# Kernel tuning notes

Measured on AMD Instinct MI355X. Metric: run time of the kernel, lower is better.

Reference implementation:

```python
import jax, jax.numpy as jnp
import numpy as np


def setup_inputs() -> dict:
    key = jax.random.key(0)
    ks = jax.random.split(key, 6)
    B, C, H, W = 4, 256, 64, 64
    C8 = C // 8
    s = 0.05
    return {
        "x": jax.random.normal(ks[0], (B, C, H, W), dtype=jnp.float32),
        "Wf": jax.random.normal(ks[1], (C8, C), dtype=jnp.float32) * s,
        "bf": jnp.zeros((C8,), dtype=jnp.float32),
        "Wg": jax.random.normal(ks[2], (C8, C), dtype=jnp.float32) * s,
        "bg": jnp.zeros((C8,), dtype=jnp.float32),
        "Wh": jax.random.normal(ks[3], (C, C), dtype=jnp.float32) * s,
        "bh": jnp.zeros((C,), dtype=jnp.float32),
        "gamma": jnp.ones((1,), dtype=jnp.float32),
    }


def reference(x, Wf, bf, Wg, bg, Wh, bh, gamma):
    B, C, H, W = x.shape
    N = H * W
    xf = x.reshape(B, C, N)  # [B, C, N] (1x1 conv == matmul over channels)
    f = jnp.einsum("kc,bcn->bkn", Wf, xf) + bf[None, :, None]  # [B, C/8, N]
    g = jnp.einsum("kc,bcn->bkn", Wg, xf) + bg[None, :, None]  # [B, C/8, N]
    h = jnp.einsum("oc,bcn->bon", Wh, xf) + bh[None, :, None]  # [B, C, N]
    # attention_map[b, n, m] = sum_k f[b,k,n] * g[b,k,m]  (f^T g)
    attn = jnp.einsum("bkn,bkm->bnm", f, g)  # [B, N, N]
    # softmax over dim -2 (the f-position axis), as in the torch module
    attn = jax.nn.softmax(attn, axis=-2)
    # out[b,c,m] = sum_n h[b,c,n] * attn[b,n,m]
    out = jnp.einsum("bcn,bnm->bcm", h, attn).reshape(B, C, H, W)
    return gamma * out + x
```

## Files before the change

### kernel.cpp

```cpp
#include <hip/hip_runtime.h>
#include <hip/hip_bf16.h>
#include <hip/hip_fp16.h>

typedef __attribute__((ext_vector_type(8))) short short8;
typedef __attribute__((ext_vector_type(8))) _Float16 half8;
typedef __attribute__((ext_vector_type(4))) float f32x4;
typedef __attribute__((ext_vector_type(16))) float f32x16;
typedef __attribute__((ext_vector_type(4))) unsigned int uint4v;
typedef unsigned short u16;
typedef unsigned int u32;

#define LOG2E 1.44269504088896f

typedef const void __attribute__((address_space(1))) gvoid;
typedef void __attribute__((address_space(3))) lvoid;

__device__ __forceinline__ void gll16(const void* g, void* l) {
  __builtin_amdgcn_global_load_lds((gvoid*)g, (lvoid*)l, 16, 0, 0);
}

__device__ __forceinline__ u16 f2bf(float f) {
  u32 u = __builtin_bit_cast(u32, f);
  u += 0x7fffu + ((u >> 16) & 1u);
  return (u16)(u >> 16);
}
__device__ __forceinline__ u16 f2h(float f) {
  _Float16 h = (_Float16)f;
  return __builtin_bit_cast(u16, h);
}
__device__ __forceinline__ u32 cvtpk_bf16(float lo, float hi) {
  u32 r;
  asm("v_cvt_pk_bf16_f32 %0, %1, %2" : "=v"(r) : "v"(lo), "v"(hi));
  return r;
}

__global__ void k_prep(const float* __restrict__ x,
                       const float* __restrict__ Wf, const float* __restrict__ bfp,
                       const float* __restrict__ Wg, const float* __restrict__ bgp,
                       const float* __restrict__ Wh, const float* __restrict__ bhp,
                       u16* __restrict__ xT, u16* __restrict__ Wall,
                       float* __restrict__ ball)
{
  int bid = blockIdx.x, t = threadIdx.x;
  if (bid < 1024) {
    __shared__ u16 tile[64][68];
    int b = bid >> 8, c0 = ((bid >> 6) & 3) << 6, n0 = (bid & 63) << 6;
#pragma unroll
    for (int r = 0; r < 4; ++r) {
      int cl = (t >> 4) + r * 16, nl = (t & 15) * 4;
      const float4 v = *(const float4*)&x[(size_t)(b * 256 + c0 + cl) * 4096 + n0 + nl];
      tile[cl][nl + 0] = f2h(v.x); tile[cl][nl + 1] = f2h(v.y);
      tile[cl][nl + 2] = f2h(v.z); tile[cl][nl + 3] = f2h(v.w);
    }
    __syncthreads();
#pragma unroll
    for (int r = 0; r < 4; ++r) {
      int nl = (t >> 4) + r * 16, cl = (t & 15) * 4;
      ushort4 o;
      o.x = tile[cl + 0][nl]; o.y = tile[cl + 1][nl];
      o.z = tile[cl + 2][nl]; o.w = tile[cl + 3][nl];
      *(ushort4*)&xT[(size_t)(b * 4096 + n0 + nl) * 256 + c0 + cl] = o;
    }
  } else {
    int wb = bid - 1024;
    int e = wb * 1024 + t * 4;
    int r = e >> 8;
    const float* src = (r < 32) ? (Wf + e)
                     : (r < 64) ? (Wg + e - 32 * 256)
                                : (Wh + e - 64 * 256);
    float4 v = *(const float4*)src;
    float sc = (r >= 32 && r < 64) ? LOG2E : 1.0f;
    ushort4 o;
    o.x = f2h(v.x * sc); o.y = f2h(v.y * sc);
    o.z = f2h(v.z * sc); o.w = f2h(v.w * sc);
    *(ushort4*)&Wall[e] = o;
    if (wb == 0 && t < 80) {
#pragma unroll
      for (int i = 0; i < 4; ++i) {
        int idx = t * 4 + i;
        ball[idx] = (idx < 32) ? bfp[idx]
                  : (idx < 64) ? bgp[idx - 32] * LOG2E
                               : bhp[idx - 64];
      }
    }
  }
}

__global__ __launch_bounds__(256, 4)
void k_proj(const u16* __restrict__ xT, const u16* __restrict__ Wall,
            const float* __restrict__ ball,
            u16* __restrict__ q, u16* __restrict__ kmat, u16* __restrict__ hbf)
{
  int bid = blockIdx.x, t = threadIdx.x;
  int w = t >> 6, l = t & 63, lg = l >> 4, li = l & 15;
  f32x4 Z = {0.f, 0.f, 0.f, 0.f};
  if (bid < 256) {
    int b = bid >> 6, n0 = (bid & 63) << 6;
    int rbase = w * 16;
    half8 aw[8];
#pragma unroll
    for (int kk = 0; kk < 8; ++kk)
      aw[kk] = *(const half8*)&Wall[(rbase + li) * 256 + kk * 32 + lg * 8];
    float bias[4];
#pragma unroll
    for (int j = 0; j < 4; ++j) bias[j] = ball[rbase + 4 * lg + j];
#pragma unroll
    for (int nn = 0; nn < 4; ++nn) {
      int n = n0 + nn * 16 + li;
      f32x4 acc = Z;
#pragma unroll
      for (int kk = 0; kk < 8; ++kk) {
        half8 bx = *(const half8*)&xT[(size_t)(b * 4096 + n) * 256 + kk * 32 + lg * 8];
        acc = __builtin_amdgcn_mfma_f32_16x16x32_f16(aw[kk], bx, acc, 0, 0, 0);
      }
      ushort4 o;
      o.x = f2h(acc[0] + bias[0]); o.y = f2h(acc[1] + bias[1]);
      o.z = f2h(acc[2] + bias[2]); o.w = f2h(acc[3] + bias[3]);
      u16* dst = (rbase < 32)
               ? (kmat + (size_t)(b * 4096 + n) * 32 + rbase + 4 * lg)
               : (q    + (size_t)(b * 4096 + n) * 32 + (rbase - 32) + 4 * lg);
      *(ushort4*)dst = o;
    }
  } else {
    int hb = bid - 256;
    int b = hb >> 8, rt = (hb >> 6) & 3, n0 = (hb & 63) << 6;
    int r0 = 64 + rt * 64;
    int nbase = n0 + w * 16;
    half8 ax[8];
#pragma unroll
    for (int kk = 0; kk < 8; ++kk)
      ax[kk] = *(const half8*)&xT[(size_t)(b * 4096 + nbase + li) * 256 + kk * 32 + lg * 8];
#pragma unroll
    for (int rr = 0; rr < 4; ++rr) {
      int r = r0 + rr * 16 + li;
      f32x4 acc = Z;
#pragma unroll
      for (int kk = 0; kk < 8; ++kk) {
        half8 bw = *(const half8*)&Wall[r * 256 + kk * 32 + lg * 8];
        acc = __builtin_amdgcn_mfma_f32_16x16x32_f16(ax[kk], bw, acc, 0, 0, 0);
      }
      float bias = ball[r];
      ushort4 o;
      o.x = f2bf(acc[0] + bias); o.y = f2bf(acc[1] + bias);
      o.z = f2bf(acc[2] + bias); o.w = f2bf(acc[3] + bias);
      *(ushort4*)&hbf[(size_t)(b * 256 + r - 64) * 4096 + nbase + 4 * lg] = o;
    }
  }
}

__global__ __launch_bounds__(512, 1)
void k_attn(const u16* __restrict__ q, const u16* __restrict__ kmat,
            const u16* __restrict__ hbf, const float* __restrict__ xin,
            const float* __restrict__ gam, float* __restrict__ out)
{
  __shared__ __align__(16) char raw[74240];
  float* vsL  = (float*)(raw + 73728);
  float* invL = (float*)(raw + 73984);

  int bid = blockIdx.x, t = threadIdx.x;
  int xcd = bid & 7;
  int b = xcd >> 1;
  int mg = ((xcd & 1) << 5) | (bid >> 3);
  int m0 = mg << 6;
  int w = t >> 6, l = t & 63, l31 = l & 31, hi = l >> 5;
  int msub = w & 1, ch = (w >> 1) & 1, kh = w >> 2;
  int mb = m0 + msub * 32;
  int c0 = ch * 128;

  const u16* qb = q + (size_t)b * 4096 * 32;
  const u16* kb = kmat + (size_t)b * 4096 * 32;
  const u16* hb = hbf + (size_t)b * 256 * 4096;

  half8 qf0 = *(const half8*)&qb[(mb + l31) * 32 + hi * 8];
  half8 qf1 = *(const half8*)&qb[(mb + l31) * 32 + 16 + hi * 8];

  f32x16 Z16 = {0,0,0,0,0,0,0,0,0,0,0,0,0,0,0,0};
  f32x16 acc0 = Z16, acc1 = Z16, acc2 = Z16, acc3 = Z16;
  float vsum = 0.f;

  int wq = t & ~63;

  {
    int nt0 = 0;
#pragma unroll
    for (int i = 0; i < 4; ++i) {
      int u = i * 512 + t;
      int skh = u >> 10, sc = (u >> 2) & 255, qp = u & 3;
      int qg = qp ^ ((sc >> 1) & 3);
      const u16* src = hb + (size_t)sc * 4096 + skh * 2048 + nt0 + qg * 8;
      char* dst = raw + (i * 512 + wq) * 16;
      gll16(src, dst);
    }
    if (w < 4) {
      int u = t;
      int skh = u >> 7, row = (u >> 2) & 31, qp = u & 3;
      int qg = qp ^ (row & 3);
      const u16* src = kb + (size_t)(skh * 2048 + nt0 + row) * 32 + qg * 8;
      char* dst = raw + 65536 + wq * 16;
      gll16(src, dst);
    }
  }

  int khV = kh * 16384;
  int khK = kh * 2048;

  for (int it = 0; it < 64; ++it) {
    int buf = it & 1;
    __syncthreads();

    if (it < 63) {
      int ntn = (it + 1) * 32;
      int bufn = buf ^ 1;
#pragma unroll
      for (int i = 0; i < 4; ++i) {
        int u = i * 512 + t;
        int skh = u >> 10, sc = (u >> 2) & 255, qp = u & 3;
        int qg = qp ^ ((sc >> 1) & 3);
        const u16* src = hb + (size_t)sc * 4096 + skh * 2048 + ntn + qg * 8;
        char* dst = raw + bufn * 32768 + (i * 512 + wq) * 16;
        gll16(src, dst);
      }
      if (w < 4) {
        int u = t;
        int skh = u >> 7, row = (u >> 2) & 31, qp = u & 3;
        int qg = qp ^ (row & 3);
        const u16* src = kb + (size_t)(skh * 2048 + ntn + row) * 32 + qg * 8;
        char* dst = raw + 65536 + bufn * 4096 + wq * 16;
        gll16(src, dst);
      }
    }

    const char* kr = raw + 65536 + buf * 4096 + khK + l31 * 64;
    int sk = (l31 & 3) * 16;
    half8 k0 = *(const half8*)(kr + ((hi * 16) ^ sk));
    half8 k1 = *(const half8*)(kr + ((32 + hi * 16) ^ sk));

    f32x16 sa = __builtin_amdgcn_mfma_f32_32x32x16_f16(k0, qf0, Z16, 0, 0, 0);
    sa = __builtin_amdgcn_mfma_f32_32x32x16_f16(k1, qf1, sa, 0, 0, 0);

    const char* vbase = raw + buf * 32768 + khV;
    uint2 a0, a1;
    uint4v v00, v01, v10, v11, v20, v21, v30, v31;
    {
      const char* vr = vbase + (c0 + 0 + l31) * 64;
      int sv = (((c0 + 0 + l31) >> 1) & 3) << 1;
      a0 = *(const uint2*)(vr + ((0 + hi) ^ sv) * 8);
      a1 = *(const uint2*)(vr + ((2 + hi) ^ sv) * 8);
      v00 = (uint4v){a0.x, a0.y, a1.x, a1.y};
      a0 = *(const uint2*)(vr + ((4 + hi) ^ sv) * 8);
      a1 = *(const uint2*)(vr + ((6 + hi) ^ sv) * 8);
      v01 = (uint4v){a0.x, a0.y, a1.x, a1.y};
    }
    {
      const char* vr = vbase + (c0 + 32 + l31) * 64;
      int sv = (((c0 + 32 + l31) >> 1) & 3) << 1;
      a0 = *(const uint2*)(vr + ((0 + hi) ^ sv) * 8);
      a1 = *(const uint2*)(vr + ((2 + hi) ^ sv) * 8);
      v10 = (uint4v){a0.x, a0.y, a1.x, a1.y};
      a0 = *(const uint2*)(vr + ((4 + hi) ^ sv) * 8);
      a1 = *(const uint2*)(vr + ((6 + hi) ^ sv) * 8);
      v11 = (uint4v){a0.x, a0.y, a1.x, a1.y};
    }
    {
      const char* vr = vbase + (c0 + 64 + l31) * 64;
      int sv = (((c0 + 64 + l31) >> 1) & 3) << 1;
      a0 = *(const uint2*)(vr + ((0 + hi) ^ sv) * 8);
      a1 = *(const uint2*)(vr + ((2 + hi) ^ sv) * 8);
      v20 = (uint4v){a0.x, a0.y, a1.x, a1.y};
      a0 = *(const uint2*)(vr + ((4 + hi) ^ sv) * 8);
      a1 = *(const uint2*)(vr + ((6 + hi) ^ sv) * 8);
      v21 = (uint4v){a0.x, a0.y, a1.x, a1.y};
    }
    {
      const char* vr = vbase + (c0 + 96 + l31) * 64;
      int sv = (((c0 + 96 + l31) >> 1) & 3) << 1;
      a0 = *(const uint2*)(vr + ((0 + hi) ^ sv) * 8);
      a1 = *(const uint2*)(vr + ((2 + hi) ^ sv) * 8);
      v30 = (uint4v){a0.x, a0.y, a1.x, a1.y};
      a0 = *(const uint2*)(vr + ((4 + hi) ^ sv) * 8);
      a1 = *(const uint2*)(vr + ((6 + hi) ^ sv) * 8);
      v31 = (uint4v){a0.x, a0.y, a1.x, a1.y};
    }

    float p[16];
#pragma unroll
    for (int r = 0; r < 16; ++r) p[r] = __builtin_amdgcn_exp2f(sa[r]);
    float s0 = 0.f, s1 = 0.f;
#pragma unroll
    for (int r = 0; r < 16; r += 2) { s0 += p[r]; s1 += p[r + 1]; }
    vsum += s0 + s1;
    u32 pk[8];
#pragma unroll
    for (int i = 0; i < 8; ++i) pk[i] = cvtpk_bf16(p[2 * i], p[2 * i + 1]);
    uint4v pa0u = {pk[0], pk[1], pk[2], pk[3]};
    uint4v pa1u = {pk[4], pk[5], pk[6], pk[7]};
    short8 pa0 = __builtin_bit_cast(short8, pa0u);
    short8 pa1 = __builtin_bit_cast(short8, pa1u);

    __builtin_amdgcn_s_setprio(1);
    acc0 = __builtin_amdgcn_mfma_f32_32x32x16_bf16(pa0, __builtin_bit_cast(short8, v00), acc0, 0, 0, 0);
    acc0 = __builtin_amdgcn_mfma_f32_32x32x16_bf16(pa1, __builtin_bit_cast(short8, v01), acc0, 0, 0, 0);
    acc1 = __builtin_amdgcn_mfma_f32_32x32x16_bf16(pa0, __builtin_bit_cast(short8, v10), acc1, 0, 0, 0);
    acc1 = __builtin_amdgcn_mfma_f32_32x32x16_bf16(pa1, __builtin_bit_cast(short8, v11), acc1, 0, 0, 0);
    acc2 = __builtin_amdgcn_mfma_f32_32x32x16_bf16(pa0, __builtin_bit_cast(short8, v20), acc2, 0, 0, 0);
    acc2 = __builtin_amdgcn_mfma_f32_32x32x16_bf16(pa1, __builtin_bit_cast(short8, v21), acc2, 0, 0, 0);
    acc3 = __builtin_amdgcn_mfma_f32_32x32x16_bf16(pa0, __builtin_bit_cast(short8, v30), acc3, 0, 0, 0);
    acc3 = __builtin_amdgcn_mfma_f32_32x32x16_bf16(pa1, __builtin_bit_cast(short8, v31), acc3, 0, 0, 0);
    __builtin_amdgcn_s_setprio(0);
  }

  __syncthreads();
  float* accL = (float*)raw;
  f32x16 acc[4] = {acc0, acc1, acc2, acc3};
  float vt = vsum + __shfl_xor(vsum, 32);
  int region = w & 3;
  if (kh == 1) {
#pragma unroll
    for (int ct = 0; ct < 4; ++ct)
#pragma unroll
      for (int g = 0; g < 4; ++g) {
        int j4 = ct * 4 + g;
        float4 v4 = {acc[ct][4 * g], acc[ct][4 * g + 1],
                     acc[ct][4 * g + 2], acc[ct][4 * g + 3]};
        *(float4*)&accL[region * 4096 + l * 64 + ((j4 ^ (l & 15)) * 4)] = v4;
      }
    if (ch == 0 && l < 32) vsL[msub * 32 + l31] = vt;
  }
  __syncthreads();
  if (kh == 0) {
#pragma unroll
    for (int ct = 0; ct < 4; ++ct)
#pragma unroll
      for (int g = 0; g < 4; ++g) {
        int j4 = ct * 4 + g;
        float4 v4 = *(const float4*)&accL[region * 4096 + l * 64 + ((j4 ^ (l & 15)) * 4)];
        acc[ct][4 * g] += v4.x; acc[ct][4 * g + 1] += v4.y;
        acc[ct][4 * g + 2] += v4.z; acc[ct][4 * g + 3] += v4.w;
      }
    if (ch == 0 && l < 32)
      invL[msub * 32 + l31] = 1.0f / (vt + vsL[msub * 32 + l31]);
  }
  __syncthreads();
  if (kh == 0) {
    float gamma = gam[0];
    const float* xb = xin + (size_t)b * 256 * 4096;
    float* ob = out + (size_t)b * 256 * 4096;
#pragma unroll
    for (int g = 0; g < 4; ++g) {
      float4 inv4 = *(const float4*)&invL[msub * 32 + 8 * g + 4 * hi];
#pragma unroll
      for (int ct = 0; ct < 4; ++ct) {
        int c = c0 + ct * 32 + l31;
        size_t base = (size_t)c * 4096 + mb + 8 * g + 4 * hi;
        float4 xv = *(const float4*)&xb[base];
        float4 ov;
        ov.x = gamma * acc[ct][4 * g + 0] * inv4.x + xv.x;
        ov.y = gamma * acc[ct][4 * g + 1] * inv4.y + xv.y;
        ov.z = gamma * acc[ct][4 * g + 2] * inv4.z + xv.z;
        ov.w = gamma * acc[ct][4 * g + 3] * inv4.w + xv.w;
        *(float4*)&ob[base] = ov;
      }
    }
  }
}

extern "C" void kernel_launch(void* const* d_in, const int* in_sizes, int n_in,
                              void* d_out, int out_size, void* d_ws, size_t ws_size,
                              hipStream_t stream)
{
  const float* x   = (const float*)d_in[0];
  const float* Wf  = (const float*)d_in[1];
  const float* bfp = (const float*)d_in[2];
  const float* Wg  = (const float*)d_in[3];
  const float* bgp = (const float*)d_in[4];
  const float* Wh  = (const float*)d_in[5];
  const float* bhp = (const float*)d_in[6];
  const float* gam = (const float*)d_in[7];
  float* out = (float*)d_out;

  char* ws = (char*)d_ws;
  u16*   xT   = (u16*)(ws);
  u16*   Wall = (u16*)(ws + 8388608);
  float* ball = (float*)(ws + 8552448);
  u16*   q    = (u16*)(ws + 8554496);
  u16*   km   = (u16*)(ws + 10651648);
  u16*   hbf  = (u16*)(ws + 12748800);

  k_prep<<<dim3(1104), dim3(256), 0, stream>>>(x, Wf, bfp, Wg, bgp, Wh, bhp, xT, Wall, ball);
  k_proj<<<dim3(1280), dim3(256), 0, stream>>>(xT, Wall, ball, q, km, hbf);
  k_attn<<<dim3(256),  dim3(512), 0, stream>>>(q, km, hbf, x, gam, out);
}
```

Baseline: 136.8 us.

## Restructure attention kernel to 32-query blocks with full key sweep, no split-K

The attention kernel now launches 512 blocks of 256 threads, each owning 32 query positions and sweeping all 4096 keys. Each of its four waves covers 64 output channels. This drops the two-way key split and its shared-memory cross-wave reduction, halves LDS use and allows several blocks per CU for higher occupancy. In exchange, each block streams the full V and K tiles for fewer queries, so V traffic per query doubles and the score MFMA and exp work are repeated across the four waves.

```diff
diff --git a/kernel.cpp b/kernel.cpp
--- a/kernel.cpp
+++ b/kernel.cpp
@@ -148,89 +148,79 @@
   }
 }
 
-__global__ __launch_bounds__(512, 1)
+__global__ __launch_bounds__(256, 4)
 void k_attn(const u16* __restrict__ q, const u16* __restrict__ kmat,
             const u16* __restrict__ hbf, const float* __restrict__ xin,
             const float* __restrict__ gam, float* __restrict__ out)
 {
-  __shared__ __align__(16) char raw[74240];
-  float* vsL  = (float*)(raw + 73728);
-  float* invL = (float*)(raw + 73984);
+  __shared__ __align__(16) char raw[36992];
+  float* invL = (float*)(raw + 36864);
 
   int bid = blockIdx.x, t = threadIdx.x;
   int xcd = bid & 7;
   int b = xcd >> 1;
-  int mg = ((xcd & 1) << 5) | (bid >> 3);
-  int m0 = mg << 6;
+  int mg = ((xcd & 1) << 6) | (bid >> 3);
+  int m0 = mg << 5;
   int w = t >> 6, l = t & 63, l31 = l & 31, hi = l >> 5;
-  int msub = w & 1, ch = (w >> 1) & 1, kh = w >> 2;
-  int mb = m0 + msub * 32;
-  int c0 = ch * 128;
+  int c0 = w * 64;
+  int wq = t & ~63;
 
   const u16* qb = q + (size_t)b * 4096 * 32;
   const u16* kb = kmat + (size_t)b * 4096 * 32;
   const u16* hb = hbf + (size_t)b * 256 * 4096;
 
-  half8 qf0 = *(const half8*)&qb[(mb + l31) * 32 + hi * 8];
-  half8 qf1 = *(const half8*)&qb[(mb + l31) * 32 + 16 + hi * 8];
+  half8 qf0 = *(const half8*)&qb[(m0 + l31) * 32 + hi * 8];
+  half8 qf1 = *(const half8*)&qb[(m0 + l31) * 32 + 16 + hi * 8];
 
   f32x16 Z16 = {0,0,0,0,0,0,0,0,0,0,0,0,0,0,0,0};
-  f32x16 acc0 = Z16, acc1 = Z16, acc2 = Z16, acc3 = Z16;
+  f32x16 acc0 = Z16, acc1 = Z16;
   float vsum = 0.f;
 
-  int wq = t & ~63;
-
   {
-    int nt0 = 0;
 #pragma unroll
     for (int i = 0; i < 4; ++i) {
-      int u = i * 512 + t;
-      int skh = u >> 10, sc = (u >> 2) & 255, qp = u & 3;
+      int u = i * 256 + t;
+      int sc = u >> 2, qp = u & 3;
       int qg = qp ^ ((sc >> 1) & 3);
-      const u16* src = hb + (size_t)sc * 4096 + skh * 2048 + nt0 + qg * 8;
-      char* dst = raw + (i * 512 + wq) * 16;
+      const u16* src = hb + (size_t)sc * 4096 + 0 + qg * 8;
+      char* dst = raw + (i * 256 + wq) * 16;
       gll16(src, dst);
     }
-    if (w < 4) {
-      int u = t;
-      int skh = u >> 7, row = (u >> 2) & 31, qp = u & 3;
+    if (t < 128) {
+      int row = t >> 2, qp = t & 3;
       int qg = qp ^ (row & 3);
-      const u16* src = kb + (size_t)(skh * 2048 + nt0 + row) * 32 + qg * 8;
-      char* dst = raw + 65536 + wq * 16;
+      const u16* src = kb + (size_t)(0 + row) * 32 + qg * 8;
+      char* dst = raw + 32768 + wq * 16;
       gll16(src, dst);
     }
   }
 
-  int khV = kh * 16384;
-  int khK = kh * 2048;
-
-  for (int it = 0; it < 64; ++it) {
+  for (int it = 0; it < 128; ++it) {
     int buf = it & 1;
     __syncthreads();
 
-    if (it < 63) {
+    if (it < 127) {
       int ntn = (it + 1) * 32;
       int bufn = buf ^ 1;
 #pragma unroll
       for (int i = 0; i < 4; ++i) {
-        int u = i * 512 + t;
-        int skh = u >> 10, sc = (u >> 2) & 255, qp = u & 3;
+        int u = i * 256 + t;
+        int sc = u >> 2, qp = u & 3;
         int qg = qp ^ ((sc >> 1) & 3);
-        const u16* src = hb + (size_t)sc * 4096 + skh * 2048 + ntn + qg * 8;
-        char* dst = raw + bufn * 32768 + (i * 512 + wq) * 16;
+        const u16* src = hb + (size_t)sc * 4096 + ntn + qg * 8;
+        char* dst = raw + bufn * 16384 + (i * 256 + wq) * 16;
         gll16(src, dst);
       }
-      if (w < 4) {
-        int u = t;
-        int skh = u >> 7, row = (u >> 2) & 31, qp = u & 3;
+      if (t < 128) {
+        int row = t >> 2, qp = t & 3;
         int qg = qp ^ (row & 3);
-        const u16* src = kb + (size_t)(skh * 2048 + ntn + row) * 32 + qg * 8;
-        char* dst = raw + 65536 + bufn * 4096 + wq * 16;
+        const u16* src = kb + (size_t)(ntn + row) * 32 + qg * 8;
+        char* dst = raw + 32768 + bufn * 2048 + wq * 16;
         gll16(src, dst);
       }
     }
 
-    const char* kr = raw + 65536 + buf * 4096 + khK + l31 * 64;
+    const char* kr = raw + 32768 + buf * 2048 + l31 * 64;
     int sk = (l31 & 3) * 16;
     half8 k0 = *(const half8*)(kr + ((hi * 16) ^ sk));
     half8 k1 = *(const half8*)(kr + ((32 + hi * 16) ^ sk));
@@ -238,9 +228,9 @@
     f32x16 sa = __builtin_amdgcn_mfma_f32_32x32x16_f16(k0, qf0, Z16, 0, 0, 0);
     sa = __builtin_amdgcn_mfma_f32_32x32x16_f16(k1, qf1, sa, 0, 0, 0);
 
-    const char* vbase = raw + buf * 32768 + khV;
+    const char* vbase = raw + buf * 16384;
     uint2 a0, a1;
-    uint4v v00, v01, v10, v11, v20, v21, v30, v31;
+    uint4v v00, v01, v10, v11;
     {
       const char* vr = vbase + (c0 + 0 + l31) * 64;
       int sv = (((c0 + 0 + l31) >> 1) & 3) << 1;
@@ -261,26 +251,6 @@
       a1 = *(const uint2*)(vr + ((6 + hi) ^ sv) * 8);
       v11 = (uint4v){a0.x, a0.y, a1.x, a1.y};
     }
-    {
-      const char* vr = vbase + (c0 + 64 + l31) * 64;
-      int sv = (((c0 + 64 + l31) >> 1) & 3) << 1;
-      a0 = *(const uint2*)(vr + ((0 + hi) ^ sv) * 8);
-      a1 = *(const uint2*)(vr + ((2 + hi) ^ sv) * 8);
-      v20 = (uint4v){a0.x, a0.y, a1.x, a1.y};
-      a0 = *(const uint2*)(vr + ((4 + hi) ^ sv) * 8);
-      a1 = *(const uint2*)(vr + ((6 + hi) ^ sv) * 8);
-      v21 = (uint4v){a0.x, a0.y, a1.x, a1.y};
-    }
-    {
-      const char* vr = vbase + (c0 + 96 + l31) * 64;
-      int sv = (((c0 + 96 + l31) >> 1) & 3) << 1;
-      a0 = *(const uint2*)(vr + ((0 + hi) ^ sv) * 8);
-      a1 = *(const uint2*)(vr + ((2 + hi) ^ sv) * 8);
-      v30 = (uint4v){a0.x, a0.y, a1.x, a1.y};
-      a0 = *(const uint2*)(vr + ((4 + hi) ^ sv) * 8);
-      a1 = *(const uint2*)(vr + ((6 + hi) ^ sv) * 8);
-      v31 = (uint4v){a0.x, a0.y, a1.x, a1.y};
-    }
 
     float p[16];
 #pragma unroll
@@ -302,56 +272,24 @@
     acc0 = __builtin_amdgcn_mfma_f32_32x32x16_bf16(pa1, __builtin_bit_cast(short8, v01), acc0, 0, 0, 0);
     acc1 = __builtin_amdgcn_mfma_f32_32x32x16_bf16(pa0, __builtin_bit_cast(short8, v10), acc1, 0, 0, 0);
     acc1 = __builtin_amdgcn_mfma_f32_32x32x16_bf16(pa1, __builtin_bit_cast(short8, v11), acc1, 0, 0, 0);
-    acc2 = __builtin_amdgcn_mfma_f32_32x32x16_bf16(pa0, __builtin_bit_cast(short8, v20), acc2, 0, 0, 0);
-    acc2 = __builtin_amdgcn_mfma_f32_32x32x16_bf16(pa1, __builtin_bit_cast(short8, v21), acc2, 0, 0, 0);
-    acc3 = __builtin_amdgcn_mfma_f32_32x32x16_bf16(pa0, __builtin_bit_cast(short8, v30), acc3, 0, 0, 0);
-    acc3 = __builtin_amdgcn_mfma_f32_32x32x16_bf16(pa1, __builtin_bit_cast(short8, v31), acc3, 0, 0, 0);
     __builtin_amdgcn_s_setprio(0);
   }
 
+  float vt = vsum + __shfl_xor(vsum, 32);
+  if (w == 0 && l < 32) invL[l31] = 1.0f / vt;
   __syncthreads();
-  float* accL = (float*)raw;
-  f32x16 acc[4] = {acc0, acc1, acc2, acc3};
-  float vt = vsum + __shfl_xor(vsum, 32);
-  int region = w & 3;
-  if (kh == 1) {
-#pragma unroll
-    for (int ct = 0; ct < 4; ++ct)
-#pragma unroll
-      for (int g = 0; g < 4; ++g) {
-        int j4 = ct * 4 + g;
-        float4 v4 = {acc[ct][4 * g], acc[ct][4 * g + 1],
-                     acc[ct][4 * g + 2], acc[ct][4 * g + 3]};
-        *(float4*)&accL[region * 4096 + l * 64 + ((j4 ^ (l & 15)) * 4)] = v4;
-      }
-    if (ch == 0 && l < 32) vsL[msub * 32 + l31] = vt;
-  }
-  __syncthreads();
-  if (kh == 0) {
-#pragma unroll
-    for (int ct = 0; ct < 4; ++ct)
-#pragma unroll
-      for (int g = 0; g < 4; ++g) {
-        int j4 = ct * 4 + g;
-        float4 v4 = *(const float4*)&accL[region * 4096 + l * 64 + ((j4 ^ (l & 15)) * 4)];
-        acc[ct][4 * g] += v4.x; acc[ct][4 * g + 1] += v4.y;
-        acc[ct][4 * g + 2] += v4.z; acc[ct][4 * g + 3] += v4.w;
-      }
-    if (ch == 0 && l < 32)
-      invL[msub * 32 + l31] = 1.0f / (vt + vsL[msub * 32 + l31]);
-  }
-  __syncthreads();
-  if (kh == 0) {
+  {
     float gamma = gam[0];
     const float* xb = xin + (size_t)b * 256 * 4096;
     float* ob = out + (size_t)b * 256 * 4096;
+    f32x16 acc[2] = {acc0, acc1};
 #pragma unroll
     for (int g = 0; g < 4; ++g) {
-      float4 inv4 = *(const float4*)&invL[msub * 32 + 8 * g + 4 * hi];
-#pragma unroll
-      for (int ct = 0; ct < 4; ++ct) {
+      float4 inv4 = *(const float4*)&invL[8 * g + 4 * hi];
+#pragma unroll
+      for (int ct = 0; ct < 2; ++ct) {
         int c = c0 + ct * 32 + l31;
-        size_t base = (size_t)c * 4096 + mb + 8 * g + 4 * hi;
+        size_t base = (size_t)c * 4096 + m0 + 8 * g + 4 * hi;
         float4 xv = *(const float4*)&xb[base];
         float4 ov;
         ov.x = gamma * acc[ct][4 * g + 0] * inv4.x + xv.x;
@@ -388,5 +326,5 @@
 
   k_prep<<<dim3(1104), dim3(256), 0, stream>>>(x, Wf, bfp, Wg, bgp, Wh, bhp, xT, Wall, ball);
   k_proj<<<dim3(1280), dim3(256), 0, stream>>>(xT, Wall, ball, q, km, hbf);
-  k_attn<<<dim3(256),  dim3(512), 0, stream>>>(q, km, hbf, x, gam, out);
-}
+  k_attn<<<dim3(512),  dim3(256), 0, stream>>>(q, km, hbf, x, gam, out);
+}
```

Result: faster. 133.0 us (-2.8%).
